# Optimization experiments

Measured on AMD Instinct MI355X. Metric: run time of the kernel, lower is better.

Reference implementation:

```python
import jax, jax.numpy as jnp
import numpy as np

H = 256            # hidden_size
S = 4              # num_of_steps
B = 512            # reactions
N_MOLS = B * S     # 2048 molecules
ATOMS_PER_MOL = 32
N_ATOMS = N_MOLS * ATOMS_PER_MOL   # 65536
BONDS_PER_MOL = 64
N_BONDS = N_MOLS * BONDS_PER_MOL   # 131072 directed bonds (+1 pad row)
MAX_NB = 6
ATOM_FDIM = 133
BOND_FDIM = 147
DEPTH = 3
N_ITERS = 3  # Set2Set iterations


def setup_inputs() -> dict:
    key = jax.random.key(0)
    ks = jax.random.split(key, 20)
    def p(k, shape):
        return jax.random.normal(k, shape, jnp.float32) * 0.02
    inp = {}
    inp['f_atoms'] = jax.random.normal(ks[0], (N_ATOMS, ATOM_FDIM), jnp.float32)
    f_bonds = jax.random.normal(ks[1], (N_BONDS + 1, BOND_FDIM), jnp.float32)
    inp['f_bonds'] = f_bonds.at[0].set(0.0)  # chemprop zero pad row
    inp['a2b'] = jax.random.randint(ks[2], (N_ATOMS, MAX_NB), 0, N_BONDS + 1)
    inp['b2a'] = jax.random.randint(ks[3], (N_BONDS + 1,), 0, N_ATOMS)
    inp['b2revb'] = jax.random.randint(ks[4], (N_BONDS + 1,), 0, N_BONDS + 1)
    # MPN weights (bias=False for W_i/W_h as in args.bias default)
    inp['W_i'] = p(ks[5], (BOND_FDIM, H))
    inp['W_h'] = p(ks[6], (H, H))
    inp['W_o'] = p(ks[7], (ATOM_FDIM + H, H)); inp['b_o'] = jnp.zeros((H,), jnp.float32)
    # NNAttention over steps
    inp['W_nn0'] = p(ks[8], (2 * H, H));  inp['b_nn0'] = jnp.zeros((H,), jnp.float32)
    inp['W_nn0s'] = p(ks[9], (H, H));     inp['b_nn0s'] = jnp.zeros((H,), jnp.float32)
    inp['W_nn1'] = p(ks[10], (S * H, H)); inp['b_nn1'] = jnp.zeros((H,), jnp.float32)
    # node Set2Set (LSTM: input 2H -> hidden H) + condenser
    inp['lstm_n_Wih'] = p(ks[11], (4 * H, 2 * H))
    inp['lstm_n_Whh'] = p(ks[12], (4 * H, H))
    inp['lstm_n_b'] = jnp.zeros((4 * H,), jnp.float32)
    inp['node_cond_W'] = p(ks[13], (2 * H, H)); inp['node_cond_b'] = jnp.zeros((H,), jnp.float32)
    # graph (step) Set2Set + condenser
    inp['lstm_g_Wih'] = p(ks[14], (4 * H, 2 * H))
    inp['lstm_g_Whh'] = p(ks[15], (4 * H, H))
    inp['lstm_g_b'] = jnp.zeros((4 * H,), jnp.float32)
    inp['graph_cond_W'] = p(ks[16], (2 * H, H)); inp['graph_cond_b'] = jnp.zeros((H,), jnp.float32)
    return inp


def set2set(feat, Wih, Whh, b):
    # feat: [M, N, D]; LSTM n_layers=1, PyTorch gate order i,f,g,o
    M, N, D = feat.shape
    h = jnp.zeros((M, D), feat.dtype)
    c = jnp.zeros((M, D), feat.dtype)
    q_star = jnp.zeros((M, 2 * D), feat.dtype)
    for _ in range(N_ITERS):
        gates = q_star @ Wih.T + h @ Whh.T + b
        i, f, g, o = jnp.split(gates, 4, axis=-1)
        c = jax.nn.sigmoid(f) * c + jax.nn.sigmoid(i) * jnp.tanh(g)
        h = jax.nn.sigmoid(o) * jnp.tanh(c)
        q = h
        alpha = jax.nn.softmax(jnp.einsum('md,mnd->mn', q, feat), axis=1)
        readout = jnp.einsum('mn,mnd->md', alpha, feat)
        q_star = jnp.concatenate([q, readout], axis=-1)
    return q_star


def nn_attention(h, W0, b0, W0s, b0s, W1, b1):
    # vectorized form of the Attention module's s1/s2 double loop
    Bm, Sm, D = h.shape
    h1 = jnp.broadcast_to(h[:, :, None, :], (Bm, Sm, Sm, D))
    h2 = jnp.broadcast_to(h[:, None, :, :], (Bm, Sm, Sm, D))
    pair = jnp.concatenate([h1, h2], -1) @ W0 + b0          # [B,S,S,D] NN0(cat(h_s1,h_s2))
    self_o = h @ W0s + b0s                                   # [B,S,D]   NN0_self(h_s1)
    diag = jnp.eye(Sm, dtype=bool)[None, :, :, None]
    out = jnp.where(diag, self_o[:, :, None, :], pair)       # diagonal uses NN0_self
    return out.reshape(Bm, Sm, Sm * D) @ W1 + b1             # NN1 over s2-concat


def reference(f_atoms, f_bonds, a2b, b2a, b2revb, W_i, W_h, W_o, b_o,
              W_nn0, b_nn0, W_nn0s, b_nn0s, W_nn1, b_nn1,
              lstm_n_Wih, lstm_n_Whh, lstm_n_b, node_cond_W, node_cond_b,
              lstm_g_Wih, lstm_g_Whh, lstm_g_b, graph_cond_W, graph_cond_b):
    # --- bond message passing (chemprop, atom_messages=False) ---
    inp = f_bonds @ W_i                       # [NB+1, H], row 0 = 0 (no bias)
    message = jax.nn.relu(inp)
    message = message.at[0].set(0.0)          # keep pad row zero
    for _ in range(DEPTH - 1):
        a_message = message[a2b].sum(axis=1)          # gather+sum: [NA, H]
        msg = a_message[b2a] - message[b2revb]        # [NB+1, H]
        message = jax.nn.relu(inp + msg @ W_h)
        message = message.at[0].set(0.0)
    nei = message[a2b].sum(axis=1)                    # [NA, H]
    atom_h = jax.nn.relu(jnp.concatenate([f_atoms, nei], -1) @ W_o + b_o)
    # --- node readout: Set2Set per molecule + condenser ---
    feat = atom_h.reshape(N_MOLS, ATOMS_PER_MOL, H)
    mol = set2set(feat, lstm_n_Wih, lstm_n_Whh, lstm_n_b) @ node_cond_W + node_cond_b
    # --- step attention (NNAttention over num_of_steps) ---
    steps = mol.reshape(B, S, H)
    steps = nn_attention(steps, W_nn0, b_nn0, W_nn0s, b_nn0s, W_nn1, b_nn1)
    # --- step readout: Set2Set over steps + condenser ---
    out = set2set(steps, lstm_g_Wih, lstm_g_Whh, lstm_g_b) @ graph_cond_W + graph_cond_b
    return out  # [B, H]
```

## Files before the change

### kernel.cpp

```cpp
#include <hip/hip_runtime.h>
#include <math.h>

#define H 256
#define S_STEPS 4
#define B_RXN 512
#define N_MOLS 2048
#define ATOMS_PER_MOL 32
#define N_ATOMS 65536
#define N_BONDS 131072
#define NBP1 131073
#define MAX_NB 6
#define ATOM_FDIM 133
#define BOND_FDIM 147
#define DEPTH 3
#define N_ITERS 3

typedef unsigned short bf16u;
typedef __attribute__((ext_vector_type(8))) short short8v;
typedef __attribute__((ext_vector_type(4))) float f32x4;

__device__ __forceinline__ float b2f(bf16u u) {
    union { unsigned int i; float f; } c; c.i = ((unsigned int)u) << 16; return c.f;
}
__device__ __forceinline__ bf16u f2b(float f) {
    union { float f; unsigned int i; } c; c.f = f;
    unsigned int i = c.i;
    return (bf16u)((i + 0x7FFFu + ((i >> 16) & 1u)) >> 16);
}
__device__ __forceinline__ unsigned int relu2bf(unsigned int w) {
    unsigned int lo = w & 0xFFFFu, hi = w >> 16;
    if (lo & 0x8000u) lo = 0u;
    if (hi & 0x8000u) hi = 0u;
    return lo | (hi << 16);
}

template<int MODE, bool RELUA>
__global__ __launch_bounds__(512) void dense_gemm_k(
    const bf16u* __restrict__ A1,
    const bf16u* __restrict__ A2,
    const bf16u* __restrict__ WT,
    const float* __restrict__ bias,
    bf16u* __restrict__ outb,
    int M)
{
    constexpr int KP = (MODE == 0) ? 160 : ((MODE == 1) ? 256 : 416);
    __shared__ bf16u As[128][40];
    __shared__ bf16u Bs[256][40];

    const int tid = threadIdx.x;
    const int lane = tid & 63, w = tid >> 6;
    const int wr = w >> 2, wc = w & 3;
    const int m0 = blockIdx.x * 128;
    const int ar = tid >> 2, q8 = (tid & 3) * 8;
    const int br = tid >> 1, bh = (tid & 1) * 16;
    const int arow = m0 + ar;
    const bool rok = arow < M;
    const int lr = lane & 15, lk = (lane >> 4) * 8;
    const uint4 z4 = {0u, 0u, 0u, 0u};

    f32x4 acc[4][4];
    const f32x4 zf = {0.f, 0.f, 0.f, 0.f};
    #pragma unroll
    for (int i = 0; i < 4; ++i)
        #pragma unroll
        for (int j = 0; j < 4; ++j) acc[i][j] = zf;

    for (int k0 = 0; k0 < KP; k0 += 32) {
        const int kc = k0 + q8;
        uint4 va;
        if (MODE == 2) {
            va = (kc < 160) ? *(const uint4*)(A1 + (size_t)arow * 160 + kc)
                            : *(const uint4*)(A2 + (size_t)arow * 256 + (kc - 160));
        } else {
            constexpr int LDA = (MODE == 0) ? 160 : 256;
            va = rok ? *(const uint4*)(A1 + (size_t)arow * LDA + kc) : z4;
        }
        if (RELUA) {
            va.x = relu2bf(va.x); va.y = relu2bf(va.y);
            va.z = relu2bf(va.z); va.w = relu2bf(va.w);
        }
        *(uint4*)&As[ar][q8] = va;
        {
            const bf16u* bp = WT + (size_t)br * KP + k0 + bh;
            uint4 b0 = *(const uint4*)(bp);
            uint4 b1 = *(const uint4*)(bp + 8);
            *(uint4*)&Bs[br][bh] = b0;
            *(uint4*)&Bs[br][bh + 8] = b1;
        }
        __syncthreads();

        short8v a[4], b[4];
        #pragma unroll
        for (int mf = 0; mf < 4; ++mf)
            a[mf] = *(const short8v*)&As[wr * 64 + mf * 16 + lr][lk];
        #pragma unroll
        for (int nf = 0; nf < 4; ++nf)
            b[nf] = *(const short8v*)&Bs[wc * 64 + nf * 16 + lr][lk];
        #pragma unroll
        for (int mf = 0; mf < 4; ++mf)
            #pragma unroll
            for (int nf = 0; nf < 4; ++nf)
                acc[mf][nf] = __builtin_amdgcn_mfma_f32_16x16x32_bf16(
                    a[mf], b[nf], acc[mf][nf], 0, 0, 0);
        __syncthreads();
    }

    const int rbase = (lane >> 4) * 4;
    #pragma unroll
    for (int mf = 0; mf < 4; ++mf) {
        #pragma unroll
        for (int nf = 0; nf < 4; ++nf) {
            const int col = wc * 64 + nf * 16 + lr;
            #pragma unroll
            for (int r = 0; r < 4; ++r) {
                const int row = m0 + wr * 64 + mf * 16 + rbase + r;
                if (row >= M) continue;
                float v = acc[mf][nf][r];
                const size_t off = (size_t)row * H + col;
                if (MODE == 2) {
                    v += bias[col];
                    outb[off] = f2b(fmaxf(v, 0.f));
                } else {
                    outb[off] = f2b(v);
                }
            }
        }
    }
}

__global__ __launch_bounds__(256) void combine_k(
    const bf16u* __restrict__ inp, const bf16u* __restrict__ AP,
    const bf16u* __restrict__ MW,
    const int* __restrict__ b2a, const int* __restrict__ b2revb,
    bf16u* __restrict__ msg)
{
    int idx = blockIdx.x * 256 + threadIdx.x;
    if (idx >= NBP1 * 32) return;
    int b = idx >> 5, c = (idx & 31) * 8;
    bf16u* op = msg + (size_t)b * H + c;
    if (b == 0) {
        *(uint4*)op = make_uint4(0u, 0u, 0u, 0u);
        return;
    }
    int a = b2a[b], rb = b2revb[b];
    uint4 ui = *(const uint4*)(inp + (size_t)b * H + c);
    uint4 up = *(const uint4*)(AP + (size_t)a * H + c);
    uint4 um = *(const uint4*)(MW + (size_t)rb * H + c);
    uint4 o;
    unsigned int* pi = &ui.x; unsigned int* pp = &up.x;
    unsigned int* pm = &um.x; unsigned int* po = &o.x;
    #pragma unroll
    for (int t = 0; t < 4; ++t) {
        float lo = b2f((bf16u)(pi[t] & 0xFFFFu)) + b2f((bf16u)(pp[t] & 0xFFFFu))
                 - b2f((bf16u)(pm[t] & 0xFFFFu));
        float hi = b2f((bf16u)(pi[t] >> 16)) + b2f((bf16u)(pp[t] >> 16))
                 - b2f((bf16u)(pm[t] >> 16));
        lo = fmaxf(lo, 0.f); hi = fmaxf(hi, 0.f);
        po[t] = (unsigned int)f2b(lo) | ((unsigned int)f2b(hi) << 16);
    }
    *(uint4*)op = o;
}

template<bool BIAS>
__global__ __launch_bounds__(256) void lin64_k(
    const float* __restrict__ A1, int lda1, int KA1,
    const float* __restrict__ A2, int lda2,
    const bf16u* __restrict__ WT, int ldw,
    const float* __restrict__ bias,
    float* __restrict__ C, int ldc, int K)
{
    __shared__ bf16u As[64][72];
    __shared__ bf16u Bs[64][72];
    const int tid = threadIdx.x;
    const int lane = tid & 63, w = tid >> 6;
    const int m0 = blockIdx.x * 64;
    const int col0 = blockIdx.y * 64;
    const int ar = tid >> 2, kq8 = (tid & 3) * 8;
    const int lr = lane & 15, lk = (lane >> 4) * 8;

    f32x4 acc[4];
    const f32x4 zf = {0.f, 0.f, 0.f, 0.f};
    #pragma unroll
    for (int j = 0; j < 4; ++j) acc[j] = zf;

    for (int k0 = 0; k0 < K; k0 += 64) {
        const float* srcA = (k0 < KA1)
            ? (A1 + (size_t)(m0 + ar) * lda1 + k0)
            : (A2 + (size_t)(m0 + ar) * lda2 + (k0 - KA1));
        #pragma unroll
        for (int hh = 0; hh < 2; ++hh) {
            const float* p = srcA + hh * 32 + kq8;
            float4 f0 = *(const float4*)p;
            float4 f1 = *(const float4*)(p + 4);
            ushort4 s0, s1;
            s0.x = f2b(f0.x); s0.y = f2b(f0.y); s0.z = f2b(f0.z); s0.w = f2b(f0.w);
            s1.x = f2b(f1.x); s1.y = f2b(f1.y); s1.z = f2b(f1.z); s1.w = f2b(f1.w);
            *(ushort4*)&As[ar][hh * 32 + kq8] = s0;
            *(ushort4*)&As[ar][hh * 32 + kq8 + 4] = s1;
            *(uint4*)&Bs[ar][hh * 32 + kq8] =
                *(const uint4*)(WT + (size_t)(col0 + ar) * ldw + k0 + hh * 32 + kq8);
        }
        __syncthreads();

        short8v a0 = *(const short8v*)&As[w * 16 + lr][lk];
        short8v a1 = *(const short8v*)&As[w * 16 + lr][32 + lk];
        #pragma unroll
        for (int nf = 0; nf < 4; ++nf) {
            short8v b0 = *(const short8v*)&Bs[nf * 16 + lr][lk];
            acc[nf] = __builtin_amdgcn_mfma_f32_16x16x32_bf16(a0, b0, acc[nf], 0, 0, 0);
        }
        #pragma unroll
        for (int nf = 0; nf < 4; ++nf) {
            short8v b1 = *(const short8v*)&Bs[nf * 16 + lr][32 + lk];
            acc[nf] = __builtin_amdgcn_mfma_f32_16x16x32_bf16(a1, b1, acc[nf], 0, 0, 0);
        }
        __syncthreads();
    }

    const int rbase = (lane >> 4) * 4;
    #pragma unroll
    for (int nf = 0; nf < 4; ++nf) {
        const int col = col0 + nf * 16 + lr;
        #pragma unroll
        for (int r = 0; r < 4; ++r) {
            const int row = m0 + w * 16 + rbase + r;
            float v = acc[nf][r];
            if (BIAS) v += bias[col];
            C[(size_t)row * ldc + col] = v;
        }
    }
}

__device__ __forceinline__ float sigm(float x) { return 1.f / (1.f + expf(-x)); }

__global__ __launch_bounds__(256) void gates_lstm_k(
    const float* __restrict__ QSTAR,
    const float* __restrict__ Hc,
    const float* __restrict__ Cc,
    const bf16u* __restrict__ WT,
    const float* __restrict__ bias,
    float* __restrict__ Hn,
    float* __restrict__ Cn,
    int M)
{
    __shared__ bf16u As[64][72];
    __shared__ bf16u Bs[64][72];
    const int tid = threadIdx.x;
    const int lane = tid & 63, w = tid >> 6;
    const int m0 = blockIdx.x * 64;
    const int db = blockIdx.y;
    const int ar = tid >> 2, q8 = (tid & 3) * 8;
    const int lr = lane & 15, lk = (lane >> 4) * 8;

    f32x4 acc[4];
    const f32x4 zf = {0.f, 0.f, 0.f, 0.f};
    #pragma unroll
    for (int g = 0; g < 4; ++g) acc[g] = zf;

    const int rho = tid >> 2;
    const int bg = rho >> 4, bcn = rho & 15;

    for (int k0 = 0; k0 < 768; k0 += 64) {
        const float* srcA = (k0 < 512)
            ? QSTAR + (size_t)(m0 + ar) * 512 + k0
            : Hc + (size_t)(m0 + ar) * 256 + (k0 - 512);
        #pragma unroll
        for (int hh = 0; hh < 2; ++hh) {
            const float* p = srcA + hh * 32 + q8;
            float4 f0 = *(const float4*)p;
            float4 f1 = *(const float4*)(p + 4);
            ushort4 s0, s1;
            s0.x = f2b(f0.x); s0.y = f2b(f0.y); s0.z = f2b(f0.z); s0.w = f2b(f0.w);
            s1.x = f2b(f1.x); s1.y = f2b(f1.y); s1.z = f2b(f1.z); s1.w = f2b(f1.w);
            *(ushort4*)&As[ar][hh * 32 + q8] = s0;
            *(ushort4*)&As[ar][hh * 32 + q8 + 4] = s1;
            *(uint4*)&Bs[rho][hh * 32 + q8] =
                *(const uint4*)(WT + (size_t)(bg * 256 + db * 16 + bcn) * 768 + k0 + hh * 32 + q8);
        }
        __syncthreads();
        short8v a0 = *(const short8v*)&As[w * 16 + lr][lk];
        short8v a1 = *(const short8v*)&As[w * 16 + lr][32 + lk];
        #pragma unroll
        for (int g = 0; g < 4; ++g) {
            short8v b0 = *(const short8v*)&Bs[g * 16 + lr][lk];
            acc[g] = __builtin_amdgcn_mfma_f32_16x16x32_bf16(a0, b0, acc[g], 0, 0, 0);
        }
        #pragma unroll
        for (int g = 0; g < 4; ++g) {
            short8v b1 = *(const short8v*)&Bs[g * 16 + lr][32 + lk];
            acc[g] = __builtin_amdgcn_mfma_f32_16x16x32_bf16(a1, b1, acc[g], 0, 0, 0);
        }
        __syncthreads();
    }

    const int rbase = (lane >> 4) * 4;
    const int d = db * 16 + lr;
    const float bi = bias[d], bf = bias[256 + d], bg_ = bias[512 + d], bo = bias[768 + d];
    #pragma unroll
    for (int r = 0; r < 4; ++r) {
        const int row = m0 + w * 16 + rbase + r;
        float i_ = acc[0][r] + bi;
        float f_ = acc[1][r] + bf;
        float g_ = acc[2][r] + bg_;
        float o_ = acc[3][r] + bo;
        float cv = sigm(f_) * Cc[(size_t)row * 256 + d] + sigm(i_) * tanhf(g_);
        Cn[(size_t)row * 256 + d] = cv;
        Hn[(size_t)row * 256 + d] = sigm(o_) * tanhf(cv);
    }
}

__global__ __launch_bounds__(256) void lstm0_bcast_k(const float* __restrict__ bias,
                                                     float* __restrict__ Hn,
                                                     float* __restrict__ Cn, int M)
{
    int idx = blockIdx.x * 256 + threadIdx.x;
    if (idx >= M * 256) return;
    int d = idx & 255;
    float c0 = sigm(bias[d]) * tanhf(bias[512 + d]);
    float h0 = sigm(bias[768 + d]) * tanhf(c0);
    Cn[idx] = c0;
    Hn[idx] = h0;
}

__global__ __launch_bounds__(256) void prep_wt_k(const float* __restrict__ W,
                                                 bf16u* __restrict__ WT, int K, int KP)
{
    int idx = blockIdx.x * 256 + threadIdx.x;
    if (idx >= 256 * KP) return;
    int n = idx / KP, k = idx - n * KP;
    WT[idx] = (k < K) ? f2b(W[(size_t)k * H + n]) : (bf16u)0;
}

__global__ __launch_bounds__(256) void prep_wto_k(const float* __restrict__ Wo,
                                                  bf16u* __restrict__ WT)
{
    int idx = blockIdx.x * 256 + threadIdx.x;
    if (idx >= 256 * 416) return;
    int n = idx / 416, k = idx - n * 416;
    float v = 0.f;
    if (k < ATOM_FDIM) v = Wo[(size_t)k * H + n];
    else if (k >= 160) v = Wo[(size_t)(ATOM_FDIM + k - 160) * H + n];
    WT[idx] = f2b(v);
}

#define SZ_WTG   786432
#define SZ_WTNC  131072
#define SZ_WTPQS 196608
#define SZ_WTN1  262144
#define SZ_WTGC  131072
__global__ __launch_bounds__(256) void prep_mid_k(
    const float* __restrict__ Wih_n, const float* __restrict__ Whh_n,
    const float* __restrict__ Wih_g, const float* __restrict__ Whh_g,
    const float* __restrict__ ncW,  const float* __restrict__ Wnn0,
    const float* __restrict__ Wnn0s, const float* __restrict__ Wnn1,
    const float* __restrict__ gcW,  const float* __restrict__ b_nn0s,
    bf16u* __restrict__ WTG_N, bf16u* __restrict__ WTG_G,
    bf16u* __restrict__ WT_NC, bf16u* __restrict__ WT_PQS,
    bf16u* __restrict__ WT_N1, bf16u* __restrict__ WT_GC,
    float* __restrict__ BIAS_PQS)
{
    int idx = blockIdx.x * 256 + threadIdx.x;
    if (idx < SZ_WTG) {
        int n = idx / 768, k = idx - n * 768;
        WTG_N[idx] = f2b(k < 512 ? Wih_n[(size_t)n * 512 + k] : Whh_n[(size_t)n * 256 + (k - 512)]);
        return;
    }
    idx -= SZ_WTG;
    if (idx < SZ_WTG) {
        int n = idx / 768, k = idx - n * 768;
        WTG_G[idx] = f2b(k < 512 ? Wih_g[(size_t)n * 512 + k] : Whh_g[(size_t)n * 256 + (k - 512)]);
        return;
    }
    idx -= SZ_WTG;
    if (idx < SZ_WTNC) {
        int n = idx / 512, k = idx - n * 512;
        WT_NC[idx] = f2b(ncW[(size_t)k * 256 + n]);
        return;
    }
    idx -= SZ_WTNC;
    if (idx < SZ_WTPQS) {
        int n = idx / 256, k = idx - n * 256;
        float v;
        if (n < 256)      v = Wnn0[(size_t)k * 256 + n];
        else if (n < 512) v = Wnn0[(size_t)(256 + k) * 256 + (n - 256)];
        else              v = Wnn0s[(size_t)k * 256 + (n - 512)];
        WT_PQS[idx] = f2b(v);
        return;
    }
    idx -= SZ_WTPQS;
    if (idx < SZ_WTN1) {
        int n = idx / 1024, k = idx - n * 1024;
        WT_N1[idx] = f2b(Wnn1[(size_t)k * 256 + n]);
        return;
    }
    idx -= SZ_WTN1;
    if (idx < SZ_WTGC) {
        int n = idx / 512, k = idx - n * 512;
        WT_GC[idx] = f2b(gcW[(size_t)k * 256 + n]);
        return;
    }
    idx -= SZ_WTGC;
    if (idx < 768) BIAS_PQS[idx] = (idx < 512) ? 0.f : b_nn0s[idx - 512];
}
#define PREP_MID_TOTAL (2 * SZ_WTG + SZ_WTNC + SZ_WTPQS + SZ_WTN1 + SZ_WTGC + 768)

__global__ __launch_bounds__(256) void prep_feat16_k(const float* __restrict__ F,
                                                     bf16u* __restrict__ O,
                                                     int rows, int K)
{
    int idx = blockIdx.x * 256 + threadIdx.x;
    if (idx >= rows * 40) return;
    int r = idx / 40, c4 = (idx - r * 40) * 4;
    const float* src = F + (size_t)r * K + c4;
    ushort4 o;
    o.x = (c4 + 0 < K) ? f2b(src[0]) : (bf16u)0;
    o.y = (c4 + 1 < K) ? f2b(src[1]) : (bf16u)0;
    o.z = (c4 + 2 < K) ? f2b(src[2]) : (bf16u)0;
    o.w = (c4 + 3 < K) ? f2b(src[3]) : (bf16u)0;
    *(ushort4*)(O + (size_t)r * 160 + c4) = o;
}

__global__ __launch_bounds__(256) void gather6_bf16_k(const bf16u* __restrict__ msg,
                                                      const int* __restrict__ a2b,
                                                      bf16u* __restrict__ outb)
{
    int idx = blockIdx.x * 256 + threadIdx.x;
    if (idx >= N_ATOMS * (H / 8)) return;
    int na = idx >> 5, c = idx & 31;
    const int* nb = a2b + (size_t)na * MAX_NB;
    float s[8] = {0.f, 0.f, 0.f, 0.f, 0.f, 0.f, 0.f, 0.f};
    #pragma unroll
    for (int j = 0; j < MAX_NB; ++j) {
        uint4 u = *(const uint4*)(msg + (size_t)nb[j] * H + c * 8);
        s[0] += b2f((bf16u)(u.x & 0xFFFFu)); s[1] += b2f((bf16u)(u.x >> 16));
        s[2] += b2f((bf16u)(u.y & 0xFFFFu)); s[3] += b2f((bf16u)(u.y >> 16));
        s[4] += b2f((bf16u)(u.z & 0xFFFFu)); s[5] += b2f((bf16u)(u.z >> 16));
        s[6] += b2f((bf16u)(u.w & 0xFFFFu)); s[7] += b2f((bf16u)(u.w >> 16));
    }
    uint4 o;
    o.x = (unsigned int)f2b(s[0]) | ((unsigned int)f2b(s[1]) << 16);
    o.y = (unsigned int)f2b(s[2]) | ((unsigned int)f2b(s[3]) << 16);
    o.z = (unsigned int)f2b(s[4]) | ((unsigned int)f2b(s[5]) << 16);
    o.w = (unsigned int)f2b(s[6]) | ((unsigned int)f2b(s[7]) << 16);
    *(uint4*)(outb + (size_t)na * H + c * 8) = o;
}

template<bool BF16F>
__global__ __launch_bounds__(256) void s2s_attn_k(const void* __restrict__ featv,
                                                  const float* __restrict__ h,
                                                  float* __restrict__ q_star, int Nn)
{
    int m = blockIdx.x;
    int t = threadIdx.x;
    int lane = t & 63, wave = t >> 6;
    __shared__ float sc[32];
    const bf16u* fb = (const bf16u*)featv;
    const float* ff = (const float*)featv;
    const size_t fbase = (size_t)m * Nn * H;
    const float* hm = h + (size_t)m * H;
    for (int n = wave; n < Nn; n += 4) {
        float p = 0.f;
        if (BF16F) {
            ushort4 u = *(const ushort4*)(fb + fbase + (size_t)n * H + lane * 4);
            const float4 h4 = *(const float4*)(hm + lane * 4);
            p = b2f(u.x) * h4.x + b2f(u.y) * h4.y + b2f(u.z) * h4.z + b2f(u.w) * h4.w;
        } else {
            const float* fr = ff + fbase + (size_t)n * H;
            #pragma unroll
            for (int u = 0; u < 4; ++u) p += fr[lane * 4 + u] * hm[lane * 4 + u];
        }
        #pragma unroll
        for (int o = 32; o >= 1; o >>= 1) p += __shfl_xor(p, o);
        if (lane == 0) sc[n] = p;
    }
    __syncthreads();
    float mx = -1e30f;
    for (int n = 0; n < Nn; ++n) mx = fmaxf(mx, sc[n]);
    float ssum = 0.f, r = 0.f;
    for (int n = 0; n < Nn; ++n) {
        float a = expf(sc[n] - mx);
        ssum += a;
        float fv = BF16F ? b2f(fb[fbase + (size_t)n * H + t]) : ff[fbase + (size_t)n * H + t];
        r += a * fv;
    }
    r /= ssum;
    q_star[(size_t)m * (2 * H) + t] = hm[t];
    q_star[(size_t)m * (2 * H) + H + t] = r;
}

__global__ __launch_bounds__(256) void build_x_k(const float* __restrict__ PQS,
                                                 const float* __restrict__ b0,
                                                 float* __restrict__ X)
{
    int idx = blockIdx.x * 256 + threadIdx.x;
    if (idx >= B_RXN * S_STEPS * S_STEPS * H) return;
    int d  = idx & 255;
    int s2 = (idx >> 8) & 3;
    int s1 = (idx >> 10) & 3;
    int b  = idx >> 12;
    float v;
    if (s1 == s2) v = PQS[((size_t)(b * S_STEPS + s1)) * 768 + 512 + d];
    else v = PQS[((size_t)(b * S_STEPS + s1)) * 768 + d]
           + PQS[((size_t)(b * S_STEPS + s2)) * 768 + 256 + d] + b0[d];
    X[idx] = v;
}

extern "C" void kernel_launch(void* const* d_in, const int* in_sizes, int n_in,
                              void* d_out, int out_size, void* d_ws, size_t ws_size,
                              hipStream_t stream)
{
    const float* f_atoms   = (const float*)d_in[0];
    const float* f_bonds   = (const float*)d_in[1];
    const int*   a2b       = (const int*)d_in[2];
    const int*   b2a       = (const int*)d_in[3];
    const int*   b2revb    = (const int*)d_in[4];
    const float* W_i       = (const float*)d_in[5];
    const float* W_h       = (const float*)d_in[6];
    const float* W_o       = (const float*)d_in[7];
    const float* b_o       = (const float*)d_in[8];
    const float* W_nn0     = (const float*)d_in[9];
    const float* b_nn0     = (const float*)d_in[10];
    const float* W_nn0s    = (const float*)d_in[11];
    const float* b_nn0s    = (const float*)d_in[12];
    const float* W_nn1     = (const float*)d_in[13];
    const float* b_nn1     = (const float*)d_in[14];
    const float* lstm_n_Wih = (const float*)d_in[15];
    const float* lstm_n_Whh = (const float*)d_in[16];
    const float* lstm_n_b   = (const float*)d_in[17];
    const float* node_cond_W = (const float*)d_in[18];
    const float* node_cond_b = (const float*)d_in[19];
    const float* lstm_g_Wih = (const float*)d_in[20];
    const float* lstm_g_Whh = (const float*)d_in[21];
    const float* lstm_g_b   = (const float*)d_in[22];
    const float* graph_cond_W = (const float*)d_in[23];
    const float* graph_cond_b = (const float*)d_in[24];
    float* out = (float*)d_out;

    const size_t SZB = (size_t)NBP1 * H * sizeof(bf16u);
    char* base = (char*)d_ws;
    bf16u* INP  = (bf16u*)(base);
    bf16u* MSG  = (bf16u*)(base + SZB);
    bf16u* MW   = (bf16u*)(base + 2 * SZB);
    bf16u* AMSG = (bf16u*)(base + 3 * SZB);
    bf16u* WT_I = (bf16u*)(base + 3 * SZB + 33554432);
    bf16u* WT_H = (bf16u*)(base + 3 * SZB + 33636352);
    bf16u* WT_O = (bf16u*)(base + 3 * SZB + 33767424);
    bf16u* FB16 = MW;
    bf16u* FA16 = MW;
    bf16u* ATOMH16 = (bf16u*)(base);
    float* SMALL = (float*)(base + SZB);
    float* HN     = SMALL + 2097152;
    float* CN     = SMALL + 2621440;
    float* QSTARN = SMALL + 3145728;
    float* MOL    = SMALL + 4194304;
    float* PQS    = SMALL + 4718592;
    float* XBUF   = SMALL + 6291456;
    float* STEPS  = SMALL + 8388608;
    float* HG     = SMALL + 8912896;
    float* CG     = SMALL + 9043968;
    float* QSTARG = SMALL + 9175040;
    float* HN2    = SMALL + 10485760;
    float* CN2    = SMALL + 11010048;
    float* HG2    = SMALL + 11534336;
    float* CG2    = SMALL + 11665408;
    char* sm2 = base + 2 * SZB + 25165824;
    bf16u* WTG_N   = (bf16u*)(sm2);
    bf16u* WTG_G   = (bf16u*)(sm2 + 1572864);
    bf16u* WT_NC   = (bf16u*)(sm2 + 3145728);
    bf16u* WT_PQS  = (bf16u*)(sm2 + 3407872);
    bf16u* WT_N1   = (bf16u*)(sm2 + 3801088);
    bf16u* WT_GC   = (bf16u*)(sm2 + 4325376);
    float* BIAS_PQS = (float*)(sm2 + 4587520);

    dim3 blk(256), blk5(512);
    const int MB_BOND = (NBP1 + 127) / 128;
    const int MB_ATOM = N_ATOMS / 128;
    const int G_GATH = (N_ATOMS * (H / 8) + 255) / 256;
    const int G_COMB = (NBP1 * 32 + 255) / 256;

    prep_wt_k<<<(256 * 160 + 255) / 256, blk, 0, stream>>>(W_i, WT_I, BOND_FDIM, 160);
    prep_wt_k<<<(256 * 256 + 255) / 256, blk, 0, stream>>>(W_h, WT_H, H, 256);
    prep_wto_k<<<(256 * 416 + 255) / 256, blk, 0, stream>>>(W_o, WT_O);
    prep_feat16_k<<<(int)(((size_t)NBP1 * 40 + 255) / 256), blk, 0, stream>>>(
        f_bonds, FB16, NBP1, BOND_FDIM);

    dense_gemm_k<0, false><<<MB_BOND, blk5, 0, stream>>>(
        FB16, nullptr, WT_I, nullptr, INP, NBP1);

    dense_gemm_k<1, true><<<MB_BOND, blk5, 0, stream>>>(
        INP, nullptr, WT_H, nullptr, MW, NBP1);
    gather6_bf16_k<<<G_GATH, blk, 0, stream>>>(MW, a2b, AMSG);
    combine_k<<<G_COMB, blk, 0, stream>>>(INP, AMSG, MW, b2a, b2revb, MSG);
    dense_gemm_k<1, false><<<MB_BOND, blk5, 0, stream>>>(
        MSG, nullptr, WT_H, nullptr, MW, NBP1);
    gather6_bf16_k<<<G_GATH, blk, 0, stream>>>(MW, a2b, AMSG);
    combine_k<<<G_COMB, blk, 0, stream>>>(INP, AMSG, MW, b2a, b2revb, MSG);

    gather6_bf16_k<<<G_GATH, blk, 0, stream>>>(MSG, a2b, AMSG);

    prep_feat16_k<<<(N_ATOMS * 40 + 255) / 256, blk, 0, stream>>>(
        f_atoms, FA16, N_ATOMS, ATOM_FDIM);
    prep_mid_k<<<(PREP_MID_TOTAL + 255) / 256, blk, 0, stream>>>(
        lstm_n_Wih, lstm_n_Whh, lstm_g_Wih, lstm_g_Whh,
        node_cond_W, W_nn0, W_nn0s, W_nn1, graph_cond_W, b_nn0s,
        WTG_N, WTG_G, WT_NC, WT_PQS, WT_N1, WT_GC, BIAS_PQS);

    dense_gemm_k<2, false><<<MB_ATOM, blk5, 0, stream>>>(
        FA16, AMSG, WT_O, b_o, ATOMH16, N_ATOMS);

    {
        lstm0_bcast_k<<<(N_MOLS * H + 255) / 256, blk, 0, stream>>>(lstm_n_b, HN, CN, N_MOLS);
        s2s_attn_k<true><<<N_MOLS, blk, 0, stream>>>(ATOMH16, HN, QSTARN, ATOMS_PER_MOL);
        float *hc = HN, *cc = CN, *hn = HN2, *cn = CN2;
        for (int it = 1; it < N_ITERS; ++it) {
            gates_lstm_k<<<dim3(N_MOLS / 64, 16), blk, 0, stream>>>(
                QSTARN, hc, cc, WTG_N, lstm_n_b, hn, cn, N_MOLS);
            s2s_attn_k<true><<<N_MOLS, blk, 0, stream>>>(ATOMH16, hn, QSTARN, ATOMS_PER_MOL);
            float* t;
            t = hc; hc = hn; hn = t;
            t = cc; cc = cn; cn = t;
        }
    }
    lin64_k<true><<<dim3(N_MOLS / 64, 4), blk, 0, stream>>>(
        QSTARN, 2 * H, 2 * H, QSTARN, 2 * H, WT_NC, 2 * H, node_cond_b, MOL, H, 2 * H);

    lin64_k<true><<<dim3(N_MOLS / 64, 12), blk, 0, stream>>>(
        MOL, H, H, MOL, H, WT_PQS, H, BIAS_PQS, PQS, 3 * H, H);
    build_x_k<<<(B_RXN * 16 * H) / 256, blk, 0, stream>>>(PQS, b_nn0, XBUF);
    lin64_k<true><<<dim3(N_MOLS / 64, 4), blk, 0, stream>>>(
        XBUF, S_STEPS * H, S_STEPS * H, XBUF, S_STEPS * H, WT_N1, S_STEPS * H, b_nn1,
        STEPS, H, S_STEPS * H);

    {
        lstm0_bcast_k<<<(B_RXN * H + 255) / 256, blk, 0, stream>>>(lstm_g_b, HG, CG, B_RXN);
        s2s_attn_k<false><<<B_RXN, blk, 0, stream>>>(STEPS, HG, QSTARG, S_STEPS);
        float *hc = HG, *cc = CG, *hn = HG2, *cn = CG2;
        for (int it = 1; it < N_ITERS; ++it) {
            gates_lstm_k<<<dim3(B_RXN / 64, 16), blk, 0, stream>>>(
                QSTARG, hc, cc, WTG_G, lstm_g_b, hn, cn, B_RXN);
            s2s_attn_k<false><<<B_RXN, blk, 0, stream>>>(STEPS, hn, QSTARG, S_STEPS);
            float* t;
            t = hc; hc = hn; hn = t;
            t = cc; cc = cn; cn = t;
        }
    }

    lin64_k<true><<<dim3(B_RXN / 64, 4), blk, 0, stream>>>(
        QSTARG, 2 * H, 2 * H, QSTARG, 2 * H, WT_GC, 2 * H, graph_cond_b, out, H, 2 * H);
}
```

Before: 570.2 us.

## Fuse fp32-to-bf16 feature conversion into GEMM loads and gather into combine

The bond and atom feature GEMMs now read the fp32 inputs directly and convert to bf16 while staging into shared memory, which removes the two separate prep_feat16 passes and their intermediate buffers. The per-atom neighbour gather is folded into the bond combine kernel, so each bond sums its source atom's six incoming messages in place instead of reading a precomputed atom sum. This removes kernel launches and the AMSG write/read round trip. In exchange, each bond redundantly re-gathers six rows (roughly doubling the gather traffic, since there are twice as many bonds as atoms), and the fp32 A loads are scalar and unaligned.

```diff
diff --git a/kernel.cpp b/kernel.cpp
--- a/kernel.cpp
+++ b/kernel.cpp
@@ -36,8 +36,8 @@
 
 template<int MODE, bool RELUA>
 __global__ __launch_bounds__(512) void dense_gemm_k(
+    const float* __restrict__ Af32,
     const bf16u* __restrict__ A1,
-    const bf16u* __restrict__ A2,
     const bf16u* __restrict__ WT,
     const float* __restrict__ bias,
     bf16u* __restrict__ outb,
@@ -67,19 +67,30 @@
 
     for (int k0 = 0; k0 < KP; k0 += 32) {
         const int kc = k0 + q8;
-        uint4 va;
-        if (MODE == 2) {
-            va = (kc < 160) ? *(const uint4*)(A1 + (size_t)arow * 160 + kc)
-                            : *(const uint4*)(A2 + (size_t)arow * 256 + (kc - 160));
+        if (MODE == 1) {
+            uint4 va = rok ? *(const uint4*)(A1 + (size_t)arow * 256 + kc) : z4;
+            if (RELUA) {
+                va.x = relu2bf(va.x); va.y = relu2bf(va.y);
+                va.z = relu2bf(va.z); va.w = relu2bf(va.w);
+            }
+            *(uint4*)&As[ar][q8] = va;
+        } else if (MODE == 2 && kc >= 160) {
+            *(uint4*)&As[ar][q8] = *(const uint4*)(A1 + (size_t)arow * 256 + (kc - 160));
         } else {
-            constexpr int LDA = (MODE == 0) ? 160 : 256;
-            va = rok ? *(const uint4*)(A1 + (size_t)arow * LDA + kc) : z4;
-        }
-        if (RELUA) {
-            va.x = relu2bf(va.x); va.y = relu2bf(va.y);
-            va.z = relu2bf(va.z); va.w = relu2bf(va.w);
-        }
-        *(uint4*)&As[ar][q8] = va;
+            constexpr int KF = (MODE == 0) ? BOND_FDIM : ATOM_FDIM;
+            const float* p = Af32 + (size_t)arow * KF + kc;
+            ushort4 s0, s1;
+            s0.x = (rok && kc + 0 < KF) ? f2b(p[0]) : (bf16u)0;
+            s0.y = (rok && kc + 1 < KF) ? f2b(p[1]) : (bf16u)0;
+            s0.z = (rok && kc + 2 < KF) ? f2b(p[2]) : (bf16u)0;
+            s0.w = (rok && kc + 3 < KF) ? f2b(p[3]) : (bf16u)0;
+            s1.x = (rok && kc + 4 < KF) ? f2b(p[4]) : (bf16u)0;
+            s1.y = (rok && kc + 5 < KF) ? f2b(p[5]) : (bf16u)0;
+            s1.z = (rok && kc + 6 < KF) ? f2b(p[6]) : (bf16u)0;
+            s1.w = (rok && kc + 7 < KF) ? f2b(p[7]) : (bf16u)0;
+            *(ushort4*)&As[ar][q8] = s0;
+            *(ushort4*)&As[ar][q8 + 4] = s1;
+        }
         {
             const bf16u* bp = WT + (size_t)br * KP + k0 + bh;
             uint4 b0 = *(const uint4*)(bp);
@@ -128,10 +139,10 @@
     }
 }
 
-__global__ __launch_bounds__(256) void combine_k(
-    const bf16u* __restrict__ inp, const bf16u* __restrict__ AP,
-    const bf16u* __restrict__ MW,
-    const int* __restrict__ b2a, const int* __restrict__ b2revb,
+__global__ __launch_bounds__(256) void fused_gc_k(
+    const bf16u* __restrict__ inp, const bf16u* __restrict__ MW,
+    const int* __restrict__ a2b, const int* __restrict__ b2a,
+    const int* __restrict__ b2revb,
     bf16u* __restrict__ msg)
 {
     int idx = blockIdx.x * 256 + threadIdx.x;
@@ -143,19 +154,32 @@
         return;
     }
     int a = b2a[b], rb = b2revb[b];
+    const int* nb = a2b + (size_t)a * MAX_NB;
     uint4 ui = *(const uint4*)(inp + (size_t)b * H + c);
-    uint4 up = *(const uint4*)(AP + (size_t)a * H + c);
     uint4 um = *(const uint4*)(MW + (size_t)rb * H + c);
+    float s[8];
+    const unsigned int* pi = &ui.x;
+    const unsigned int* pm = &um.x;
+    #pragma unroll
+    for (int t = 0; t < 4; ++t) {
+        s[2 * t]     = b2f((bf16u)(pi[t] & 0xFFFFu)) - b2f((bf16u)(pm[t] & 0xFFFFu));
+        s[2 * t + 1] = b2f((bf16u)(pi[t] >> 16))     - b2f((bf16u)(pm[t] >> 16));
+    }
+    #pragma unroll
+    for (int j = 0; j < MAX_NB; ++j) {
+        uint4 u = *(const uint4*)(MW + (size_t)nb[j] * H + c);
+        const unsigned int* pu = &u.x;
+        #pragma unroll
+        for (int t = 0; t < 4; ++t) {
+            s[2 * t]     += b2f((bf16u)(pu[t] & 0xFFFFu));
+            s[2 * t + 1] += b2f((bf16u)(pu[t] >> 16));
+        }
+    }
     uint4 o;
-    unsigned int* pi = &ui.x; unsigned int* pp = &up.x;
-    unsigned int* pm = &um.x; unsigned int* po = &o.x;
+    unsigned int* po = &o.x;
     #pragma unroll
     for (int t = 0; t < 4; ++t) {
-        float lo = b2f((bf16u)(pi[t] & 0xFFFFu)) + b2f((bf16u)(pp[t] & 0xFFFFu))
-                 - b2f((bf16u)(pm[t] & 0xFFFFu));
-        float hi = b2f((bf16u)(pi[t] >> 16)) + b2f((bf16u)(pp[t] >> 16))
-                 - b2f((bf16u)(pm[t] >> 16));
-        lo = fmaxf(lo, 0.f); hi = fmaxf(hi, 0.f);
+        float lo = fmaxf(s[2 * t], 0.f), hi = fmaxf(s[2 * t + 1], 0.f);
         po[t] = (unsigned int)f2b(lo) | ((unsigned int)f2b(hi) << 16);
     }
     *(uint4*)op = o;
@@ -403,22 +427,6 @@
     if (idx < 768) BIAS_PQS[idx] = (idx < 512) ? 0.f : b_nn0s[idx - 512];
 }
 #define PREP_MID_TOTAL (2 * SZ_WTG + SZ_WTNC + SZ_WTPQS + SZ_WTN1 + SZ_WTGC + 768)
-
-__global__ __launch_bounds__(256) void prep_feat16_k(const float* __restrict__ F,
-                                                     bf16u* __restrict__ O,
-                                                     int rows, int K)
-{
-    int idx = blockIdx.x * 256 + threadIdx.x;
-    if (idx >= rows * 40) return;
-    int r = idx / 40, c4 = (idx - r * 40) * 4;
-    const float* src = F + (size_t)r * K + c4;
-    ushort4 o;
-    o.x = (c4 + 0 < K) ? f2b(src[0]) : (bf16u)0;
-    o.y = (c4 + 1 < K) ? f2b(src[1]) : (bf16u)0;
-    o.z = (c4 + 2 < K) ? f2b(src[2]) : (bf16u)0;
-    o.w = (c4 + 3 < K) ? f2b(src[3]) : (bf16u)0;
-    *(ushort4*)(O + (size_t)r * 160 + c4) = o;
-}
 
 __global__ __launch_bounds__(256) void gather6_bf16_k(const bf16u* __restrict__ msg,
                                                       const int* __restrict__ a2b,
@@ -545,8 +553,6 @@
     bf16u* WT_I = (bf16u*)(base + 3 * SZB + 33554432);
     bf16u* WT_H = (bf16u*)(base + 3 * SZB + 33636352);
     bf16u* WT_O = (bf16u*)(base + 3 * SZB + 33767424);
-    bf16u* FB16 = MW;
-    bf16u* FA16 = MW;
     bf16u* ATOMH16 = (bf16u*)(base);
     float* SMALL = (float*)(base + SZB);
     float* HN     = SMALL + 2097152;
@@ -581,32 +587,26 @@
     prep_wt_k<<<(256 * 160 + 255) / 256, blk, 0, stream>>>(W_i, WT_I, BOND_FDIM, 160);
     prep_wt_k<<<(256 * 256 + 255) / 256, blk, 0, stream>>>(W_h, WT_H, H, 256);
     prep_wto_k<<<(256 * 416 + 255) / 256, blk, 0, stream>>>(W_o, WT_O);
-    prep_feat16_k<<<(int)(((size_t)NBP1 * 40 + 255) / 256), blk, 0, stream>>>(
-        f_bonds, FB16, NBP1, BOND_FDIM);
 
     dense_gemm_k<0, false><<<MB_BOND, blk5, 0, stream>>>(
-        FB16, nullptr, WT_I, nullptr, INP, NBP1);
+        f_bonds, nullptr, WT_I, nullptr, INP, NBP1);
 
     dense_gemm_k<1, true><<<MB_BOND, blk5, 0, stream>>>(
-        INP, nullptr, WT_H, nullptr, MW, NBP1);
-    gather6_bf16_k<<<G_GATH, blk, 0, stream>>>(MW, a2b, AMSG);
-    combine_k<<<G_COMB, blk, 0, stream>>>(INP, AMSG, MW, b2a, b2revb, MSG);
+        nullptr, INP, WT_H, nullptr, MW, NBP1);
+    fused_gc_k<<<G_COMB, blk, 0, stream>>>(INP, MW, a2b, b2a, b2revb, MSG);
     dense_gemm_k<1, false><<<MB_BOND, blk5, 0, stream>>>(
-        MSG, nullptr, WT_H, nullptr, MW, NBP1);
-    gather6_bf16_k<<<G_GATH, blk, 0, stream>>>(MW, a2b, AMSG);
-    combine_k<<<G_COMB, blk, 0, stream>>>(INP, AMSG, MW, b2a, b2revb, MSG);
+        nullptr, MSG, WT_H, nullptr, MW, NBP1);
+    fused_gc_k<<<G_COMB, blk, 0, stream>>>(INP, MW, a2b, b2a, b2revb, MSG);
 
     gather6_bf16_k<<<G_GATH, blk, 0, stream>>>(MSG, a2b, AMSG);
 
-    prep_feat16_k<<<(N_ATOMS * 40 + 255) / 256, blk, 0, stream>>>(
-        f_atoms, FA16, N_ATOMS, ATOM_FDIM);
     prep_mid_k<<<(PREP_MID_TOTAL + 255) / 256, blk, 0, stream>>>(
         lstm_n_Wih, lstm_n_Whh, lstm_g_Wih, lstm_g_Whh,
         node_cond_W, W_nn0, W_nn0s, W_nn1, graph_cond_W, b_nn0s,
         WTG_N, WTG_G, WT_NC, WT_PQS, WT_N1, WT_GC, BIAS_PQS);
 
     dense_gemm_k<2, false><<<MB_ATOM, blk5, 0, stream>>>(
-        FA16, AMSG, WT_O, b_o, ATOMH16, N_ATOMS);
+        f_atoms, AMSG, WT_O, b_o, ATOMH16, N_ATOMS);
 
     {
         lstm0_bcast_k<<<(N_MOLS * H + 255) / 256, blk, 0, stream>>>(lstm_n_b, HN, CN, N_MOLS);
```

Result: slower. 620.3 us (+8.8%).
